# Optimization experiments

Hardware: AMD Instinct MI355X
Metric: run time of the kernel (lower is better)

## Reference

```python
import jax, jax.numpy as jnp
import numpy as np

DIM = 384
WS = 8        # window_size
SHIFT = 4     # shift_size
HEADS = 8
HEAD_DIM = DIM // HEADS
SCALE = HEAD_DIM ** (-0.5)
EPS = 1e-5


def layernorm(x, g, b):
    m = jnp.mean(x, axis=-1, keepdims=True)
    v = jnp.var(x, axis=-1, keepdims=True)
    return (x - m) * jax.lax.rsqrt(v + EPS) * g + b


def setup_inputs() -> dict:
    key = jax.random.key(0)
    ks = jax.random.split(key, 8)
    s = 0.02
    return {
        "x": jax.random.normal(ks[0], (8, DIM, 64, 64), dtype=jnp.float32),
        "qkv_w": jax.random.normal(ks[1], (DIM, 3 * DIM), dtype=jnp.float32) * s,
        "qkv_b": jnp.zeros((3 * DIM,), jnp.float32),
        "proj_w": jax.random.normal(ks[2], (DIM, DIM), dtype=jnp.float32) * s,
        "proj_b": jnp.zeros((DIM,), jnp.float32),
        "ln1_g": jnp.ones((DIM,), jnp.float32),
        "ln1_b": jnp.zeros((DIM,), jnp.float32),
        "ln2_g": jnp.ones((DIM,), jnp.float32),
        "ln2_b": jnp.zeros((DIM,), jnp.float32),
        "mlp_w1": jax.random.normal(ks[3], (DIM, 4 * DIM), dtype=jnp.float32) * s,
        "mlp_b1": jnp.zeros((4 * DIM,), jnp.float32),
        "mlp_w2": jax.random.normal(ks[4], (4 * DIM, DIM), dtype=jnp.float32) * s,
        "mlp_b2": jnp.zeros((DIM,), jnp.float32),
    }


def reference(x, qkv_w, qkv_b, proj_w, proj_b, ln1_g, ln1_b, ln2_g, ln2_b,
              mlp_w1, mlp_b1, mlp_w2, mlp_b2):
    B, C, H, W = x.shape
    x_skip = jnp.transpose(x, (0, 2, 3, 1))  # [B,H,W,C]
    xh = x_skip
    pad_b = (-H) % WS
    pad_r = (-W) % WS
    xh = jnp.pad(xh, ((0, 0), (0, pad_b), (0, pad_r), (0, 0)))
    Hp, Wp = xh.shape[1], xh.shape[2]
    if SHIFT > 0:
        xh = jnp.roll(xh, (-SHIFT, -SHIFT), axis=(1, 2))
    # window partition -> [B*nH*nW, WS*WS, C]
    win = xh.reshape(B, Hp // WS, WS, Wp // WS, WS, C)
    win = win.transpose(0, 1, 3, 2, 4, 5).reshape(-1, WS * WS, C)
    win = layernorm(win, ln1_g, ln1_b)
    # windowed MHA (no shift mask in original module)
    Bw, N, _ = win.shape
    qkv = (win @ qkv_w + qkv_b).reshape(Bw, N, 3, HEADS, HEAD_DIM)
    qkv = qkv.transpose(2, 0, 3, 1, 4)  # [3, Bw, H, N, d]
    q, k, v = qkv[0] * SCALE, qkv[1], qkv[2]
    attn = jax.nn.softmax(jnp.einsum('bhnd,bhmd->bhnm', q, k), axis=-1)
    out = jnp.einsum('bhnm,bhmd->bhnd', attn, v)
    out = out.transpose(0, 2, 1, 3).reshape(Bw, N, C)
    out = out @ proj_w + proj_b
    # window reverse
    xh = out.reshape(B, Hp // WS, Wp // WS, WS, WS, C)
    xh = xh.transpose(0, 1, 3, 2, 4, 5).reshape(B, Hp, Wp, C)
    if SHIFT > 0:
        xh = jnp.roll(xh, (SHIFT, SHIFT), axis=(1, 2))
    xh = xh[:, :H, :W, :] + x_skip
    h = layernorm(xh, ln2_g, ln2_b)
    h = jax.nn.gelu(h @ mlp_w1 + mlp_b1, approximate=False) @ mlp_w2 + mlp_b2
    return jnp.transpose(h, (0, 3, 1, 2))  # [B,C,H,W]
```

## Files before the change

kernel.cpp:

```cpp
#include <hip/hip_runtime.h>
#include <hip/hip_bf16.h>
#include <math.h>

#define DIM   384
#define HEADS 8
#define HD    48
#define NTOK  32768
#define NWIN  512

typedef __attribute__((ext_vector_type(8))) short bf16x8;
typedef __attribute__((ext_vector_type(8))) unsigned short u16x8;
typedef __attribute__((ext_vector_type(4))) float f32x4;

__device__ __forceinline__ float bf2f(unsigned short u) {
    unsigned int v = ((unsigned int)u) << 16;
    return __uint_as_float(v);
}
__device__ __forceinline__ unsigned short f2bf(float f) {
    __bf16 b = (__bf16)f;
    return __builtin_bit_cast(unsigned short, b);
}

__device__ __forceinline__ float gelu(float v) {
    float z  = v * 0.70710678118654752f;
    float az = fabsf(z);
    float t  = __builtin_amdgcn_rcpf(1.0f + 0.47047f * az);
    float p  = t * (0.3480242f + t * (-0.0958798f + t * 0.7478556f));
    float ea = 1.0f - p * __expf(-az * az);
    float er = copysignf(ea, z);
    return 0.5f * v * (1.0f + er);
}

__device__ __forceinline__ void tok2src(int tok, int& b, int& hs, int& ws) {
    int bb  = tok >> 12;
    int win = (tok >> 6) & 63;
    int t   = tok & 63;
    int hi = win >> 3, wi = win & 7;
    int r  = t >> 3,  cc = t & 7;
    b  = bb;
    hs = (hi * 8 + r  + 4) & 63;
    ws = (wi * 8 + cc + 4) & 63;
}

__global__ __launch_bounds__(256) void k_wt4(const float* __restrict__ qkv_w,
                                             const float* __restrict__ proj_w,
                                             const float* __restrict__ w1,
                                             const float* __restrict__ w2,
                                             unsigned short* __restrict__ d0,
                                             unsigned short* __restrict__ d1,
                                             unsigned short* __restrict__ d2,
                                             unsigned short* __restrict__ d3) {
    __shared__ unsigned short T[64][66];
    int b = blockIdx.x;
    const float* W; unsigned short* Wt; int K, N, lt;
    if (b < 108)      { W = qkv_w;  Wt = d0; K = 384;  N = 1152; lt = b; }
    else if (b < 144) { W = proj_w; Wt = d1; K = 384;  N = 384;  lt = b - 108; }
    else if (b < 288) { W = w1;     Wt = d2; K = 384;  N = 1536; lt = b - 144; }
    else              { W = w2;     Wt = d3; K = 1536; N = 384;  lt = b - 288; }
    int tn = N >> 6;
    int k0 = (lt / tn) << 6, n0 = (lt % tn) << 6;
    int t  = threadIdx.x;
    int cl = t & 63, rw = t >> 6;
    #pragma unroll
    for (int p = 0; p < 16; p++) {
        int kk = p * 4 + rw;
        T[cl][kk] = f2bf(W[(size_t)(k0 + kk) * N + n0 + cl]);
    }
    __syncthreads();
    #pragma unroll
    for (int p = 0; p < 16; p++) {
        int nn = p * 4 + rw;
        Wt[(size_t)(n0 + nn) * K + k0 + cl] = T[nn][cl];
    }
}

__global__ __launch_bounds__(256) void k_ln1(const float* __restrict__ x,
                                             const float* __restrict__ g,
                                             const float* __restrict__ bt,
                                             unsigned short* __restrict__ ln1) {
    int blk = blockIdx.x;
    int b  = blk >> 6, hs = blk & 63;
    int t  = threadIdx.x;
    int w  = t & 63, cg = t >> 6;
    const float* row = x + (size_t)b * DIM * 4096 + hs * 64;

    float sum = 0.f, sq = 0.f;
    for (int i = 0; i < 96; i++) {
        int c = i * 4 + cg;
        float v = row[(size_t)c * 4096 + w];
        sum += v; sq += v * v;
    }
    __shared__ float red[2][4][64];
    __shared__ float mean_s[64], rstd_s[64];
    red[0][cg][w] = sum; red[1][cg][w] = sq;
    __syncthreads();
    if (t < 64) {
        float s  = red[0][0][t] + red[0][1][t] + red[0][2][t] + red[0][3][t];
        float q2 = red[1][0][t] + red[1][1][t] + red[1][2][t] + red[1][3][t];
        float mean = s * (1.0f / DIM);
        float var  = q2 * (1.0f / DIM) - mean * mean;
        mean_s[t] = mean;
        rstd_s[t] = rsqrtf(var + 1e-5f);
    }
    __syncthreads();

    int wp = t >> 2, seg = t & 3;
    int hr = (hs + 60) & 63, wr = (wp + 60) & 63;
    int tok = ((b * 8 + (hr >> 3)) * 8 + (wr >> 3)) * 64 + (hr & 7) * 8 + (wr & 7);

    __shared__ __align__(16) unsigned short tile[64][72];
    for (int chunk = 0; chunk < 6; chunk++) {
        float mean = mean_s[w], rstd = rstd_s[w];
        #pragma unroll
        for (int it = 0; it < 16; it++) {
            int cl = it * 4 + cg;
            int c  = chunk * 64 + cl;
            float v = row[(size_t)c * 4096 + w];
            tile[w][cl] = f2bf((v - mean) * rstd * g[c] + bt[c]);
        }
        __syncthreads();
        u16x8 v0 = *(const u16x8*)&tile[wp][seg * 16];
        u16x8 v1 = *(const u16x8*)&tile[wp][seg * 16 + 8];
        unsigned short* op = ln1 + (size_t)tok * DIM + chunk * 64 + seg * 16;
        *(u16x8*)op = v0;
        *(u16x8*)(op + 8) = v1;
        __syncthreads();
    }
}

template <int EPI>
__global__ __launch_bounds__(256) void k_gemm_mfma(
        const unsigned short* __restrict__ A,
        const unsigned short* __restrict__ Bt,
        const float* __restrict__ bias,
        void* __restrict__ Cout,
        const float* __restrict__ xres,
        int N, int K, int GX) {
    __shared__ __align__(16) unsigned short SH[24576];
    int tid  = threadIdx.x;
    int lane = tid & 63;
    int wave = tid >> 6;
    int wm = wave >> 1, wn = wave & 1;
    int quad = lane >> 4, l15 = lane & 15;

    int l   = blockIdx.x;
    int xcd = l & 7;
    int r_  = l >> 3;
    int bx  = r_ % GX;
    int by  = (r_ / GX) * 8 + xcd;
    int m0 = by * 128, n0 = bx * 128;

    const unsigned short* gA0 = A  + (size_t)(m0 +      lane) * K + wave * 8;
    const unsigned short* gA1 = A  + (size_t)(m0 + 64 + lane) * K + wave * 8;
    const unsigned short* gB0 = Bt + (size_t)(n0 +      lane) * K + wave * 8;
    const unsigned short* gB1 = Bt + (size_t)(n0 + 64 + lane) * K + wave * 8;

    auto stage = [&](int buf) {
        __builtin_amdgcn_global_load_lds(
            (const __attribute__((address_space(1))) void*)gA0,
            (__attribute__((address_space(3))) void*)&SH[buf * 4096 + wave * 1024],
            16, 0, 0);
        __builtin_amdgcn_global_load_lds(
            (const __attribute__((address_space(1))) void*)gA1,
            (__attribute__((address_space(3))) void*)&SH[buf * 4096 + wave * 1024 + 512],
            16, 0, 0);
        __builtin_amdgcn_global_load_lds(
            (const __attribute__((address_space(1))) void*)gB0,
            (__attribute__((address_space(3))) void*)&SH[12288 + buf * 4096 + wave * 1024],
            16, 0, 0);
        __builtin_amdgcn_global_load_lds(
            (const __attribute__((address_space(1))) void*)gB1,
            (__attribute__((address_space(3))) void*)&SH[12288 + buf * 4096 + wave * 1024 + 512],
            16, 0, 0);
        gA0 += 32; gA1 += 32; gB0 += 32; gB1 += 32;
    };

    f32x4 acc[4][4] = {};
    int nsteps = K >> 5;

    stage(0);
    stage(1);
    int cur = 0, nxt = 2;
    for (int t = 0; t < nsteps; ++t) {
        __builtin_amdgcn_s_barrier();
        if (t + 2 < nsteps) {
            stage(nxt);
            if (++nxt == 3) nxt = 0;
            asm volatile("s_waitcnt vmcnt(8)" ::: "memory");
        } else if (t + 2 == nsteps) {
            asm volatile("s_waitcnt vmcnt(4)" ::: "memory");
        } else {
            asm volatile("s_waitcnt vmcnt(0)" ::: "memory");
        }
        __builtin_amdgcn_s_barrier();

        bf16x8 af[4], bfr[4];
        #pragma unroll
        for (int r = 0; r < 4; r++)
            af[r] = *(const bf16x8*)&SH[cur * 4096 + (quad * 128 + wm * 64 + r * 16 + l15) * 8];
        #pragma unroll
        for (int r2 = 0; r2 < 4; r2++)
            bfr[r2] = *(const bf16x8*)&SH[12288 + cur * 4096 + (quad * 128 + wn * 64 + r2 * 16 + l15) * 8];
        #pragma unroll
        for (int r = 0; r < 4; r++)
            #pragma unroll
            for (int r2 = 0; r2 < 4; r2++)
                acc[r][r2] = __builtin_amdgcn_mfma_f32_16x16x32_bf16(
                                 af[r], bfr[r2], acc[r][r2], 0, 0, 0);
        if (++cur == 3) cur = 0;
    }

    if (EPI == 2 || EPI == 3) {
        #pragma unroll
        for (int r2 = 0; r2 < 4; r2++) {
            int n = n0 + wn * 64 + r2 * 16 + l15;
            float bn = bias[n];
            #pragma unroll
            for (int r = 0; r < 4; r++) {
                #pragma unroll
                for (int reg = 0; reg < 4; reg++) {
                    int m = m0 + wm * 64 + r * 16 + quad * 4 + reg;
                    float v = acc[r][r2][reg] + bn;
                    if (EPI == 2) {
                        int b, hs, ws_;
                        tok2src(m, b, hs, ws_);
                        v += xres[(((size_t)b * DIM + n) * 64 + hs) * 64 + ws_];
                        int p = (b * 64 + hs) * 64 + ws_;
                        ((float*)Cout)[(size_t)p * N + n] = v;
                    } else {
                        ((float*)Cout)[(size_t)m * N + n] = v;
                    }
                }
            }
        }
    } else if (EPI == 5) {
        float* SF = (float*)SH;
        __syncthreads();
        int b   = m0 >> 12;
        int hs0 = (m0 >> 6) & 63;
        #pragma unroll
        for (int h2 = 0; h2 < 2; h2++) {
            if (wm == h2) {
                #pragma unroll
                for (int r2 = 0; r2 < 4; r2++) {
                    int c = wn * 64 + r2 * 16 + l15;
                    float bn = bias[n0 + c];
                    #pragma unroll
                    for (int r = 0; r < 4; r++) {
                        f32x4 v4;
                        #pragma unroll
                        for (int reg = 0; reg < 4; reg++)
                            v4[reg] = acc[r][r2][reg] + bn;
                        *(f32x4*)&SF[c * 68 + r * 16 + quad * 4] = v4;
                    }
                }
            }
            __syncthreads();
            #pragma unroll
            for (int i = 0; i < 8; i++) {
                int id = tid + i * 256;
                int c  = id >> 4, ch = id & 15;
                f32x4 v = *(const f32x4*)&SF[c * 68 + ch * 4];
                float* dst = (float*)Cout + ((size_t)(b * DIM + n0 + c) * 64 + hs0 + h2) * 64;
                *(f32x4*)&dst[ch * 4] = v;
            }
            __syncthreads();
        }
    } else {
        __syncthreads();
        #pragma unroll
        for (int r2 = 0; r2 < 4; r2++) {
            int col = wn * 64 + r2 * 16 + l15;
            float bn = bias[n0 + col];
            #pragma unroll
            for (int r = 0; r < 4; r++) {
                int row0 = wm * 64 + r * 16 + quad * 4;
                #pragma unroll
                for (int reg = 0; reg < 4; reg++) {
                    int row = row0 + reg;
                    float v = acc[r][r2][reg] + bn;
                    if (EPI == 1) v = gelu(v);
                    SH[(row * 136 + col) ^ (((row >> 3) & 1) << 4)] = f2bf(v);
                }
            }
        }
        __syncthreads();
        #pragma unroll
        for (int i = 0; i < 8; i++) {
            int chunk = tid + i * 256;
            int m = chunk >> 4, nc = chunk & 15;
            int idx = (m * 136 + nc * 8) ^ (((m >> 3) & 1) << 4);
            u16x8 v = *(const u16x8*)&SH[idx];
            if (EPI == 4) {
                int n = n0 + nc * 8;
                int qi  = n / 384;
                int rem = n - qi * 384;
                int hh  = rem / 48;
                int d   = rem - hh * 48;
                *(u16x8*)&((unsigned short*)Cout)[((size_t)(qi * 8 + hh) * NTOK + m0 + m) * 48 + d] = v;
            } else {
                *(u16x8*)&((unsigned short*)Cout)[(size_t)(m0 + m) * N + n0 + nc * 8] = v;
            }
        }
    }
}

__global__ __launch_bounds__(256) void k_attn_mfma(
        const unsigned short* __restrict__ qkvh,
        unsigned short* __restrict__ attn) {
    __shared__ __align__(16) unsigned short lds[4][8064];
    int tid  = threadIdx.x;
    int lane = tid & 63;
    int wave = tid >> 6;
    int quad = lane >> 4, l15 = lane & 15;
    int win  = blockIdx.x;
    int tok0 = win * 64;
    unsigned short* VT = &lds[wave][0];
    unsigned short* P  = &lds[wave][3456];
    const float scale = 0.14433756729740643f;

    for (int hi = 0; hi < 2; hi++) {
        int h = wave + hi * 4;
        const unsigned short* qb = qkvh + ((size_t)(0 * 8 + h) * NTOK + tok0) * 48;
        const unsigned short* kb = qkvh + ((size_t)(1 * 8 + h) * NTOK + tok0) * 48;
        const unsigned short* vb = qkvh + ((size_t)(2 * 8 + h) * NTOK + tok0) * 48;

        #pragma unroll
        for (int i = 0; i < 6; i++) {
            u16x8 v = *(const u16x8*)&vb[lane * 48 + i * 8];
            #pragma unroll
            for (int j = 0; j < 8; j++)
                VT[(i * 8 + j) * 72 + lane] = v[j];
        }

        bf16x8 kf[4][2];
        #pragma unroll
        for (int ni = 0; ni < 4; ni++) {
            kf[ni][0] = *(const bf16x8*)&kb[(ni * 16 + l15) * 48 + quad * 8];
            bf16x8 z = {};
            if (quad < 2)
                z = *(const bf16x8*)&kb[(ni * 16 + l15) * 48 + 32 + quad * 8];
            kf[ni][1] = z;
        }

        f32x4 sacc[4][4] = {};
        #pragma unroll
        for (int mi = 0; mi < 4; mi++) {
            bf16x8 qf0 = *(const bf16x8*)&qb[(mi * 16 + l15) * 48 + quad * 8];
            bf16x8 qf1 = {};
            if (quad < 2)
                qf1 = *(const bf16x8*)&qb[(mi * 16 + l15) * 48 + 32 + quad * 8];
            #pragma unroll
            for (int ni = 0; ni < 4; ni++) {
                sacc[mi][ni] = __builtin_amdgcn_mfma_f32_16x16x32_bf16(qf0, kf[ni][0], sacc[mi][ni], 0, 0, 0);
                sacc[mi][ni] = __builtin_amdgcn_mfma_f32_16x16x32_bf16(qf1, kf[ni][1], sacc[mi][ni], 0, 0, 0);
            }
        }

        #pragma unroll
        for (int mi = 0; mi < 4; mi++) {
            #pragma unroll
            for (int reg = 0; reg < 4; reg++) {
                float s0 = sacc[mi][0][reg] * scale;
                float s1 = sacc[mi][1][reg] * scale;
                float s2 = sacc[mi][2][reg] * scale;
                float s3 = sacc[mi][3][reg] * scale;
                float mx = fmaxf(fmaxf(s0, s1), fmaxf(s2, s3));
                #pragma unroll
                for (int off = 1; off < 16; off <<= 1)
                    mx = fmaxf(mx, __shfl_xor(mx, off));
                float e0 = __expf(s0 - mx);
                float e1 = __expf(s1 - mx);
                float e2 = __expf(s2 - mx);
                float e3 = __expf(s3 - mx);
                float sm = e0 + e1 + e2 + e3;
                #pragma unroll
                for (int off = 1; off < 16; off <<= 1)
                    sm += __shfl_xor(sm, off);
                float inv = 1.0f / sm;
                int row = mi * 16 + quad * 4 + reg;
                P[row * 72 +  0 + l15] = f2bf(e0 * inv);
                P[row * 72 + 16 + l15] = f2bf(e1 * inv);
                P[row * 72 + 32 + l15] = f2bf(e2 * inv);
                P[row * 72 + 48 + l15] = f2bf(e3 * inv);
            }
        }

        bf16x8 vf[3][2];
        #pragma unroll
        for (int ni = 0; ni < 3; ni++)
            #pragma unroll
            for (int kt = 0; kt < 2; kt++)
                vf[ni][kt] = *(const bf16x8*)&VT[(ni * 16 + l15) * 72 + kt * 32 + quad * 8];

        #pragma unroll
        for (int mi = 0; mi < 4; mi++) {
            bf16x8 pf0 = *(const bf16x8*)&P[(mi * 16 + l15) * 72 + quad * 8];
            bf16x8 pf1 = *(const bf16x8*)&P[(mi * 16 + l15) * 72 + 32 + quad * 8];
            f32x4 o[3] = {};
            #pragma unroll
            for (int ni = 0; ni < 3; ni++) {
                o[ni] = __builtin_amdgcn_mfma_f32_16x16x32_bf16(pf0, vf[ni][0], o[ni], 0, 0, 0);
                o[ni] = __builtin_amdgcn_mfma_f32_16x16x32_bf16(pf1, vf[ni][1], o[ni], 0, 0, 0);
            }
            #pragma unroll
            for (int ni = 0; ni < 3; ni++)
                #pragma unroll
                for (int reg = 0; reg < 4; reg++) {
                    int tok = tok0 + mi * 16 + quad * 4 + reg;
                    attn[(size_t)tok * DIM + h * HD + ni * 16 + l15] = f2bf(o[ni][reg]);
                }
        }
    }
}

__global__ __launch_bounds__(64) void k_ln2(const float* __restrict__ y,
                                            const float* __restrict__ g,
                                            const float* __restrict__ bt,
                                            unsigned short* __restrict__ out) {
    int tok = blockIdx.x;
    int t   = threadIdx.x;
    const float* row = y + (size_t)tok * DIM;
    float v[6];
    float sum = 0.f, sq = 0.f;
    #pragma unroll
    for (int i = 0; i < 6; i++) {
        v[i] = row[i * 64 + t];
        sum += v[i]; sq += v[i] * v[i];
    }
    #pragma unroll
    for (int o = 32; o > 0; o >>= 1) {
        sum += __shfl_xor(sum, o, 64);
        sq  += __shfl_xor(sq, o, 64);
    }
    float mean = sum * (1.0f / DIM);
    float var  = sq * (1.0f / DIM) - mean * mean;
    float rstd = rsqrtf(var + 1e-5f);
    unsigned short* orow = out + (size_t)tok * DIM;
    #pragma unroll
    for (int i = 0; i < 6; i++) {
        int c = i * 64 + t;
        orow[c] = f2bf((v[i] - mean) * rstd * g[c] + bt[c]);
    }
}

extern "C" void kernel_launch(void* const* d_in, const int* in_sizes, int n_in,
                              void* d_out, int out_size, void* d_ws, size_t ws_size,
                              hipStream_t stream) {
    const float* x      = (const float*)d_in[0];
    const float* qkv_w  = (const float*)d_in[1];
    const float* qkv_b  = (const float*)d_in[2];
    const float* proj_w = (const float*)d_in[3];
    const float* proj_b = (const float*)d_in[4];
    const float* ln1_g  = (const float*)d_in[5];
    const float* ln1_b  = (const float*)d_in[6];
    const float* ln2_g  = (const float*)d_in[7];
    const float* ln2_b  = (const float*)d_in[8];
    const float* w1     = (const float*)d_in[9];
    const float* b1     = (const float*)d_in[10];
    const float* w2     = (const float*)d_in[11];
    const float* b2     = (const float*)d_in[12];

    char* ws = (char*)d_ws;
    unsigned short* qkv_wt  = (unsigned short*)(ws + 0);
    unsigned short* proj_wt = (unsigned short*)(ws + 884736);
    unsigned short* w1t     = (unsigned short*)(ws + 1179648);
    unsigned short* w2t     = (unsigned short*)(ws + 2359296);
    unsigned short* ln1     = (unsigned short*)(ws + 4194304);
    unsigned short* qkv     = (unsigned short*)(ws + 29360128);
    unsigned short* attn    = (unsigned short*)(ws + 104857600);
    float*          y       = (float*)(ws + 130023424);
    unsigned short* ln2     = ln1;
    unsigned short* mid     = qkv;

    k_wt4<<<432, 256, 0, stream>>>(qkv_w, proj_w, w1, w2, qkv_wt, proj_wt, w1t, w2t);
    k_ln1<<<512, 256, 0, stream>>>(x, ln1_g, ln1_b, ln1);
    k_gemm_mfma<4><<<9 * 256, 256, 0, stream>>>(ln1, qkv_wt, qkv_b, qkv, nullptr, 1152, 384, 9);
    k_attn_mfma<<<NWIN, 256, 0, stream>>>(qkv, attn);
    k_gemm_mfma<2><<<3 * 256, 256, 0, stream>>>(attn, proj_wt, proj_b, y, x, 384, 384, 3);
    k_ln2<<<NTOK, 64, 0, stream>>>(y, ln2_g, ln2_b, ln2);
    k_gemm_mfma<1><<<12 * 256, 256, 0, stream>>>(ln2, w1t, b1, mid, nullptr, 1536, 384, 12);
    k_gemm_mfma<5><<<3 * 256, 256, 0, stream>>>(mid, w2t, b2, (float*)d_out, nullptr, 384, 1536, 3);
}
```

Measured before the change: 459.1 us.

## Add 256x128 GEMM tile variant for QKV and MLP1 projections

Adds an MT template parameter so the GEMM kernel can compute a 256-row by 128-column tile per block. Each B fragment loaded from LDS is reused across twice as many MFMAs, and the grid for the QKV and MLP-up GEMMs is halved. The new path double-buffers instead of triple-buffering and keeps two accumulator sets, which raises register pressure and may lower occupancy. The two GEMMs whose epilogues do the layout transposes stay on the 128x128 path.

Result: slower. 495.3 us (+7.9%).

```diff
diff --git a/kernel.cpp b/kernel.cpp
--- a/kernel.cpp
+++ b/kernel.cpp
@@ -128,7 +128,7 @@
     }
 }
 
-template <int EPI>
+template <int EPI, int MT>
 __global__ __launch_bounds__(256) void k_gemm_mfma(
         const unsigned short* __restrict__ A,
         const unsigned short* __restrict__ Bt,
@@ -148,69 +148,13 @@
     int r_  = l >> 3;
     int bx  = r_ % GX;
     int by  = (r_ / GX) * 8 + xcd;
-    int m0 = by * 128, n0 = bx * 128;
-
-    const unsigned short* gA0 = A  + (size_t)(m0 +      lane) * K + wave * 8;
-    const unsigned short* gA1 = A  + (size_t)(m0 + 64 + lane) * K + wave * 8;
-    const unsigned short* gB0 = Bt + (size_t)(n0 +      lane) * K + wave * 8;
-    const unsigned short* gB1 = Bt + (size_t)(n0 + 64 + lane) * K + wave * 8;
-
-    auto stage = [&](int buf) {
-        __builtin_amdgcn_global_load_lds(
-            (const __attribute__((address_space(1))) void*)gA0,
-            (__attribute__((address_space(3))) void*)&SH[buf * 4096 + wave * 1024],
-            16, 0, 0);
-        __builtin_amdgcn_global_load_lds(
-            (const __attribute__((address_space(1))) void*)gA1,
-            (__attribute__((address_space(3))) void*)&SH[buf * 4096 + wave * 1024 + 512],
-            16, 0, 0);
-        __builtin_amdgcn_global_load_lds(
-            (const __attribute__((address_space(1))) void*)gB0,
-            (__attribute__((address_space(3))) void*)&SH[12288 + buf * 4096 + wave * 1024],
-            16, 0, 0);
-        __builtin_amdgcn_global_load_lds(
-            (const __attribute__((address_space(1))) void*)gB1,
-            (__attribute__((address_space(3))) void*)&SH[12288 + buf * 4096 + wave * 1024 + 512],
-            16, 0, 0);
-        gA0 += 32; gA1 += 32; gB0 += 32; gB1 += 32;
-    };
-
-    f32x4 acc[4][4] = {};
+    int m0 = by * 128 * MT, n0 = bx * 128;
+
+    f32x4 acc0[4][4] = {};
+    f32x4 acc1[4][4] = {};
     int nsteps = K >> 5;
 
-    stage(0);
-    stage(1);
-    int cur = 0, nxt = 2;
-    for (int t = 0; t < nsteps; ++t) {
-        __builtin_amdgcn_s_barrier();
-        if (t + 2 < nsteps) {
-            stage(nxt);
-            if (++nxt == 3) nxt = 0;
-            asm volatile("s_waitcnt vmcnt(8)" ::: "memory");
-        } else if (t + 2 == nsteps) {
-            asm volatile("s_waitcnt vmcnt(4)" ::: "memory");
-        } else {
-            asm volatile("s_waitcnt vmcnt(0)" ::: "memory");
-        }
-        __builtin_amdgcn_s_barrier();
-
-        bf16x8 af[4], bfr[4];
-        #pragma unroll
-        for (int r = 0; r < 4; r++)
-            af[r] = *(const bf16x8*)&SH[cur * 4096 + (quad * 128 + wm * 64 + r * 16 + l15) * 8];
-        #pragma unroll
-        for (int r2 = 0; r2 < 4; r2++)
-            bfr[r2] = *(const bf16x8*)&SH[12288 + cur * 4096 + (quad * 128 + wn * 64 + r2 * 16 + l15) * 8];
-        #pragma unroll
-        for (int r = 0; r < 4; r++)
-            #pragma unroll
-            for (int r2 = 0; r2 < 4; r2++)
-                acc[r][r2] = __builtin_amdgcn_mfma_f32_16x16x32_bf16(
-                                 af[r], bfr[r2], acc[r][r2], 0, 0, 0);
-        if (++cur == 3) cur = 0;
-    }
-
-    if (EPI == 2 || EPI == 3) {
+    auto epi_f32 = [&](const f32x4 (&acc)[4][4], int m0h) {
         #pragma unroll
         for (int r2 = 0; r2 < 4; r2++) {
             int n = n0 + wn * 64 + r2 * 16 + l15;
@@ -219,7 +163,7 @@
             for (int r = 0; r < 4; r++) {
                 #pragma unroll
                 for (int reg = 0; reg < 4; reg++) {
-                    int m = m0 + wm * 64 + r * 16 + quad * 4 + reg;
+                    int m = m0h + wm * 64 + r * 16 + quad * 4 + reg;
                     float v = acc[r][r2][reg] + bn;
                     if (EPI == 2) {
                         int b, hs, ws_;
@@ -233,40 +177,8 @@
                 }
             }
         }
-    } else if (EPI == 5) {
-        float* SF = (float*)SH;
-        __syncthreads();
-        int b   = m0 >> 12;
-        int hs0 = (m0 >> 6) & 63;
-        #pragma unroll
-        for (int h2 = 0; h2 < 2; h2++) {
-            if (wm == h2) {
-                #pragma unroll
-                for (int r2 = 0; r2 < 4; r2++) {
-                    int c = wn * 64 + r2 * 16 + l15;
-                    float bn = bias[n0 + c];
-                    #pragma unroll
-                    for (int r = 0; r < 4; r++) {
-                        f32x4 v4;
-                        #pragma unroll
-                        for (int reg = 0; reg < 4; reg++)
-                            v4[reg] = acc[r][r2][reg] + bn;
-                        *(f32x4*)&SF[c * 68 + r * 16 + quad * 4] = v4;
-                    }
-                }
-            }
-            __syncthreads();
-            #pragma unroll
-            for (int i = 0; i < 8; i++) {
-                int id = tid + i * 256;
-                int c  = id >> 4, ch = id & 15;
-                f32x4 v = *(const f32x4*)&SF[c * 68 + ch * 4];
-                float* dst = (float*)Cout + ((size_t)(b * DIM + n0 + c) * 64 + hs0 + h2) * 64;
-                *(f32x4*)&dst[ch * 4] = v;
-            }
-            __syncthreads();
-        }
-    } else {
+    };
+    auto epi_bf16 = [&](const f32x4 (&acc)[4][4], int m0h) {
         __syncthreads();
         #pragma unroll
         for (int r2 = 0; r2 < 4; r2++) {
@@ -297,11 +209,168 @@
                 int rem = n - qi * 384;
                 int hh  = rem / 48;
                 int d   = rem - hh * 48;
-                *(u16x8*)&((unsigned short*)Cout)[((size_t)(qi * 8 + hh) * NTOK + m0 + m) * 48 + d] = v;
+                *(u16x8*)&((unsigned short*)Cout)[((size_t)(qi * 8 + hh) * NTOK + m0h + m) * 48 + d] = v;
             } else {
-                *(u16x8*)&((unsigned short*)Cout)[(size_t)(m0 + m) * N + n0 + nc * 8] = v;
-            }
-        }
+                *(u16x8*)&((unsigned short*)Cout)[(size_t)(m0h + m) * N + n0 + nc * 8] = v;
+            }
+        }
+    };
+
+    if constexpr (MT == 1) {
+        const unsigned short* gA0 = A  + (size_t)(m0 +      lane) * K + wave * 8;
+        const unsigned short* gA1 = A  + (size_t)(m0 + 64 + lane) * K + wave * 8;
+        const unsigned short* gB0 = Bt + (size_t)(n0 +      lane) * K + wave * 8;
+        const unsigned short* gB1 = Bt + (size_t)(n0 + 64 + lane) * K + wave * 8;
+        auto stage = [&](int buf) {
+            __builtin_amdgcn_global_load_lds(
+                (const __attribute__((address_space(1))) void*)gA0,
+                (__attribute__((address_space(3))) void*)&SH[buf * 4096 + wave * 1024], 16, 0, 0);
+            __builtin_amdgcn_global_load_lds(
+                (const __attribute__((address_space(1))) void*)gA1,
+                (__attribute__((address_space(3))) void*)&SH[buf * 4096 + wave * 1024 + 512], 16, 0, 0);
+            __builtin_amdgcn_global_load_lds(
+                (const __attribute__((address_space(1))) void*)gB0,
+                (__attribute__((address_space(3))) void*)&SH[12288 + buf * 4096 + wave * 1024], 16, 0, 0);
+            __builtin_amdgcn_global_load_lds(
+                (const __attribute__((address_space(1))) void*)gB1,
+                (__attribute__((address_space(3))) void*)&SH[12288 + buf * 4096 + wave * 1024 + 512], 16, 0, 0);
+            gA0 += 32; gA1 += 32; gB0 += 32; gB1 += 32;
+        };
+        stage(0);
+        stage(1);
+        int cur = 0, nxt = 2;
+        for (int t = 0; t < nsteps; ++t) {
+            __builtin_amdgcn_s_barrier();
+            if (t + 2 < nsteps) {
+                stage(nxt);
+                if (++nxt == 3) nxt = 0;
+                asm volatile("s_waitcnt vmcnt(8)" ::: "memory");
+            } else if (t + 2 == nsteps) {
+                asm volatile("s_waitcnt vmcnt(4)" ::: "memory");
+            } else {
+                asm volatile("s_waitcnt vmcnt(0)" ::: "memory");
+            }
+            __builtin_amdgcn_s_barrier();
+
+            bf16x8 af[4], bfr[4];
+            #pragma unroll
+            for (int r = 0; r < 4; r++)
+                af[r] = *(const bf16x8*)&SH[cur * 4096 + (quad * 128 + wm * 64 + r * 16 + l15) * 8];
+            #pragma unroll
+            for (int r2 = 0; r2 < 4; r2++)
+                bfr[r2] = *(const bf16x8*)&SH[12288 + cur * 4096 + (quad * 128 + wn * 64 + r2 * 16 + l15) * 8];
+            #pragma unroll
+            for (int r = 0; r < 4; r++)
+                #pragma unroll
+                for (int r2 = 0; r2 < 4; r2++)
+                    acc0[r][r2] = __builtin_amdgcn_mfma_f32_16x16x32_bf16(
+                                     af[r], bfr[r2], acc0[r][r2], 0, 0, 0);
+            if (++cur == 3) cur = 0;
+        }
+    } else {
+        const unsigned short* gA0 = A  + (size_t)(m0 +       lane) * K + wave * 8;
+        const unsigned short* gA1 = A  + (size_t)(m0 +  64 + lane) * K + wave * 8;
+        const unsigned short* gA2 = A  + (size_t)(m0 + 128 + lane) * K + wave * 8;
+        const unsigned short* gA3 = A  + (size_t)(m0 + 192 + lane) * K + wave * 8;
+        const unsigned short* gB0 = Bt + (size_t)(n0 +       lane) * K + wave * 8;
+        const unsigned short* gB1 = Bt + (size_t)(n0 +  64 + lane) * K + wave * 8;
+        auto stage2 = [&](int buf) {
+            __builtin_amdgcn_global_load_lds(
+                (const __attribute__((address_space(1))) void*)gA0,
+                (__attribute__((address_space(3))) void*)&SH[buf * 8192 + wave * 2048], 16, 0, 0);
+            __builtin_amdgcn_global_load_lds(
+                (const __attribute__((address_space(1))) void*)gA1,
+                (__attribute__((address_space(3))) void*)&SH[buf * 8192 + wave * 2048 + 512], 16, 0, 0);
+            __builtin_amdgcn_global_load_lds(
+                (const __attribute__((address_space(1))) void*)gA2,
+                (__attribute__((address_space(3))) void*)&SH[buf * 8192 + wave * 2048 + 1024], 16, 0, 0);
+            __builtin_amdgcn_global_load_lds(
+                (const __attribute__((address_space(1))) void*)gA3,
+                (__attribute__((address_space(3))) void*)&SH[buf * 8192 + wave * 2048 + 1536], 16, 0, 0);
+            __builtin_amdgcn_global_load_lds(
+                (const __attribute__((address_space(1))) void*)gB0,
+                (__attribute__((address_space(3))) void*)&SH[16384 + buf * 4096 + wave * 1024], 16, 0, 0);
+            __builtin_amdgcn_global_load_lds(
+                (const __attribute__((address_space(1))) void*)gB1,
+                (__attribute__((address_space(3))) void*)&SH[16384 + buf * 4096 + wave * 1024 + 512], 16, 0, 0);
+            gA0 += 32; gA1 += 32; gA2 += 32; gA3 += 32; gB0 += 32; gB1 += 32;
+        };
+        stage2(0);
+        for (int t = 0; t < nsteps; ++t) {
+            int cur = t & 1;
+            __builtin_amdgcn_s_barrier();
+            if (t + 1 < nsteps) {
+                stage2(cur ^ 1);
+                asm volatile("s_waitcnt vmcnt(6)" ::: "memory");
+            } else {
+                asm volatile("s_waitcnt vmcnt(0)" ::: "memory");
+            }
+            __builtin_amdgcn_s_barrier();
+
+            bf16x8 a0[4], a1[4], bfr[4];
+            #pragma unroll
+            for (int r2 = 0; r2 < 4; r2++)
+                bfr[r2] = *(const bf16x8*)&SH[16384 + cur * 4096 + (quad * 128 + wn * 64 + r2 * 16 + l15) * 8];
+            #pragma unroll
+            for (int r = 0; r < 4; r++)
+                a0[r] = *(const bf16x8*)&SH[cur * 8192 + (quad * 256 + wm * 64 + r * 16 + l15) * 8];
+            #pragma unroll
+            for (int r = 0; r < 4; r++)
+                a1[r] = *(const bf16x8*)&SH[cur * 8192 + (quad * 256 + 128 + wm * 64 + r * 16 + l15) * 8];
+            #pragma unroll
+            for (int r = 0; r < 4; r++)
+                #pragma unroll
+                for (int r2 = 0; r2 < 4; r2++)
+                    acc0[r][r2] = __builtin_amdgcn_mfma_f32_16x16x32_bf16(
+                                     a0[r], bfr[r2], acc0[r][r2], 0, 0, 0);
+            #pragma unroll
+            for (int r = 0; r < 4; r++)
+                #pragma unroll
+                for (int r2 = 0; r2 < 4; r2++)
+                    acc1[r][r2] = __builtin_amdgcn_mfma_f32_16x16x32_bf16(
+                                     a1[r], bfr[r2], acc1[r][r2], 0, 0, 0);
+        }
+    }
+
+    if constexpr (EPI == 2 || EPI == 3) {
+        epi_f32(acc0, m0);
+        if constexpr (MT == 2) epi_f32(acc1, m0 + 128);
+    } else if constexpr (EPI == 5) {
+        float* SF = (float*)SH;
+        __syncthreads();
+        int b   = m0 >> 12;
+        int hs0 = (m0 >> 6) & 63;
+        #pragma unroll
+        for (int h2 = 0; h2 < 2; h2++) {
+            if (wm == h2) {
+                #pragma unroll
+                for (int r2 = 0; r2 < 4; r2++) {
+                    int c = wn * 64 + r2 * 16 + l15;
+                    float bn = bias[n0 + c];
+                    #pragma unroll
+                    for (int r = 0; r < 4; r++) {
+                        f32x4 v4;
+                        #pragma unroll
+                        for (int reg = 0; reg < 4; reg++)
+                            v4[reg] = acc0[r][r2][reg] + bn;
+                        *(f32x4*)&SF[c * 68 + r * 16 + quad * 4] = v4;
+                    }
+                }
+            }
+            __syncthreads();
+            #pragma unroll
+            for (int i = 0; i < 8; i++) {
+                int id = tid + i * 256;
+                int c  = id >> 4, ch = id & 15;
+                f32x4 v = *(const f32x4*)&SF[c * 68 + ch * 4];
+                float* dst = (float*)Cout + ((size_t)(b * DIM + n0 + c) * 64 + hs0 + h2) * 64;
+                *(f32x4*)&dst[ch * 4] = v;
+            }
+            __syncthreads();
+        }
+    } else {
+        epi_bf16(acc0, m0);
+        if constexpr (MT == 2) epi_bf16(acc1, m0 + 128);
     }
 }
 
@@ -475,10 +544,10 @@
 
     k_wt4<<<432, 256, 0, stream>>>(qkv_w, proj_w, w1, w2, qkv_wt, proj_wt, w1t, w2t);
     k_ln1<<<512, 256, 0, stream>>>(x, ln1_g, ln1_b, ln1);
-    k_gemm_mfma<4><<<9 * 256, 256, 0, stream>>>(ln1, qkv_wt, qkv_b, qkv, nullptr, 1152, 384, 9);
+    k_gemm_mfma<4, 2><<<128 * 9, 256, 0, stream>>>(ln1, qkv_wt, qkv_b, qkv, nullptr, 1152, 384, 9);
     k_attn_mfma<<<NWIN, 256, 0, stream>>>(qkv, attn);
-    k_gemm_mfma<2><<<3 * 256, 256, 0, stream>>>(attn, proj_wt, proj_b, y, x, 384, 384, 3);
+    k_gemm_mfma<2, 1><<<3 * 256, 256, 0, stream>>>(attn, proj_wt, proj_b, y, x, 384, 384, 3);
     k_ln2<<<NTOK, 64, 0, stream>>>(y, ln2_g, ln2_b, ln2);
-    k_gemm_mfma<1><<<12 * 256, 256, 0, stream>>>(ln2, w1t, b1, mid, nullptr, 1536, 384, 12);
-    k_gemm_mfma<5><<<3 * 256, 256, 0, stream>>>(mid, w2t, b2, (float*)d_out, nullptr, 384, 1536, 3);
-}
+    k_gemm_mfma<1, 2><<<128 * 12, 256, 0, stream>>>(ln2, w1t, b1, mid, nullptr, 1536, 384, 12);
+    k_gemm_mfma<5, 1><<<3 * 256, 256, 0, stream>>>(mid, w2t, b2, (float*)d_out, nullptr, 384, 1536, 3);
+}
```

## Replace 4-wave 128x128 GEMM blocks with single-wave 64x64 blocks

Applied to the files above, without the earlier changes.

Rewrites the shared GEMM kernel so each workgroup is one wavefront computing a 64x64 tile. Staging becomes double-buffered instead of triple-buffered, and all barriers are dropped, since one wave needs no cross-wave sync. The goal is to remove barrier overhead and raise the block count and occupancy. The cost is that each A/B tile loaded into LDS is reused only within a 64x64 tile, so global and L2 traffic roughly doubles, and the LDS read patterns lose their XOR swizzle.

Measured after the change: 817.6 us. +78.1%, slower.

```diff
diff --git a/kernel.cpp b/kernel.cpp
--- a/kernel.cpp
+++ b/kernel.cpp
@@ -129,18 +129,15 @@
 }
 
 template <int EPI>
-__global__ __launch_bounds__(256) void k_gemm_mfma(
+__global__ __launch_bounds__(64) void k_gemm_wave(
         const unsigned short* __restrict__ A,
         const unsigned short* __restrict__ Bt,
         const float* __restrict__ bias,
         void* __restrict__ Cout,
         const float* __restrict__ xres,
         int N, int K, int GX) {
-    __shared__ __align__(16) unsigned short SH[24576];
-    int tid  = threadIdx.x;
-    int lane = tid & 63;
-    int wave = tid >> 6;
-    int wm = wave >> 1, wn = wave & 1;
+    __shared__ __align__(16) unsigned short SH[8704];
+    int lane = threadIdx.x;
     int quad = lane >> 4, l15 = lane & 15;
 
     int l   = blockIdx.x;
@@ -148,78 +145,65 @@
     int r_  = l >> 3;
     int bx  = r_ % GX;
     int by  = (r_ / GX) * 8 + xcd;
-    int m0 = by * 128, n0 = bx * 128;
-
-    const unsigned short* gA0 = A  + (size_t)(m0 +      lane) * K + wave * 8;
-    const unsigned short* gA1 = A  + (size_t)(m0 + 64 + lane) * K + wave * 8;
-    const unsigned short* gB0 = Bt + (size_t)(n0 +      lane) * K + wave * 8;
-    const unsigned short* gB1 = Bt + (size_t)(n0 + 64 + lane) * K + wave * 8;
+    int m0 = by * 64, n0 = bx * 64;
+
+    const unsigned short* gA = A  + (size_t)(m0 + lane) * K;
+    const unsigned short* gB = Bt + (size_t)(n0 + lane) * K;
+    int k0 = 0;
 
     auto stage = [&](int buf) {
-        __builtin_amdgcn_global_load_lds(
-            (const __attribute__((address_space(1))) void*)gA0,
-            (__attribute__((address_space(3))) void*)&SH[buf * 4096 + wave * 1024],
-            16, 0, 0);
-        __builtin_amdgcn_global_load_lds(
-            (const __attribute__((address_space(1))) void*)gA1,
-            (__attribute__((address_space(3))) void*)&SH[buf * 4096 + wave * 1024 + 512],
-            16, 0, 0);
-        __builtin_amdgcn_global_load_lds(
-            (const __attribute__((address_space(1))) void*)gB0,
-            (__attribute__((address_space(3))) void*)&SH[12288 + buf * 4096 + wave * 1024],
-            16, 0, 0);
-        __builtin_amdgcn_global_load_lds(
-            (const __attribute__((address_space(1))) void*)gB1,
-            (__attribute__((address_space(3))) void*)&SH[12288 + buf * 4096 + wave * 1024 + 512],
-            16, 0, 0);
-        gA0 += 32; gA1 += 32; gB0 += 32; gB1 += 32;
+        #pragma unroll
+        for (int j = 0; j < 4; j++)
+            __builtin_amdgcn_global_load_lds(
+                (const __attribute__((address_space(1))) void*)(gA + k0 + j * 8),
+                (__attribute__((address_space(3))) void*)&SH[buf * 4096 + j * 512],
+                16, 0, 0);
+        #pragma unroll
+        for (int j = 0; j < 4; j++)
+            __builtin_amdgcn_global_load_lds(
+                (const __attribute__((address_space(1))) void*)(gB + k0 + j * 8),
+                (__attribute__((address_space(3))) void*)&SH[buf * 4096 + 2048 + j * 512],
+                16, 0, 0);
+        k0 += 32;
     };
 
     f32x4 acc[4][4] = {};
     int nsteps = K >> 5;
 
     stage(0);
-    stage(1);
-    int cur = 0, nxt = 2;
     for (int t = 0; t < nsteps; ++t) {
-        __builtin_amdgcn_s_barrier();
-        if (t + 2 < nsteps) {
-            stage(nxt);
-            if (++nxt == 3) nxt = 0;
+        int cur = t & 1;
+        if (t + 1 < nsteps) {
+            stage(cur ^ 1);
             asm volatile("s_waitcnt vmcnt(8)" ::: "memory");
-        } else if (t + 2 == nsteps) {
-            asm volatile("s_waitcnt vmcnt(4)" ::: "memory");
         } else {
             asm volatile("s_waitcnt vmcnt(0)" ::: "memory");
         }
-        __builtin_amdgcn_s_barrier();
-
         bf16x8 af[4], bfr[4];
         #pragma unroll
         for (int r = 0; r < 4; r++)
-            af[r] = *(const bf16x8*)&SH[cur * 4096 + (quad * 128 + wm * 64 + r * 16 + l15) * 8];
+            af[r] = *(const bf16x8*)&SH[cur * 4096 + quad * 512 + (r * 16 + l15) * 8];
         #pragma unroll
         for (int r2 = 0; r2 < 4; r2++)
-            bfr[r2] = *(const bf16x8*)&SH[12288 + cur * 4096 + (quad * 128 + wn * 64 + r2 * 16 + l15) * 8];
+            bfr[r2] = *(const bf16x8*)&SH[cur * 4096 + 2048 + quad * 512 + (r2 * 16 + l15) * 8];
         #pragma unroll
         for (int r = 0; r < 4; r++)
             #pragma unroll
             for (int r2 = 0; r2 < 4; r2++)
                 acc[r][r2] = __builtin_amdgcn_mfma_f32_16x16x32_bf16(
                                  af[r], bfr[r2], acc[r][r2], 0, 0, 0);
-        if (++cur == 3) cur = 0;
-    }
-
-    if (EPI == 2 || EPI == 3) {
+    }
+
+    if constexpr (EPI == 2 || EPI == 3) {
         #pragma unroll
         for (int r2 = 0; r2 < 4; r2++) {
-            int n = n0 + wn * 64 + r2 * 16 + l15;
+            int n = n0 + r2 * 16 + l15;
             float bn = bias[n];
             #pragma unroll
             for (int r = 0; r < 4; r++) {
                 #pragma unroll
                 for (int reg = 0; reg < 4; reg++) {
-                    int m = m0 + wm * 64 + r * 16 + quad * 4 + reg;
+                    int m = m0 + r * 16 + quad * 4 + reg;
                     float v = acc[r][r2][reg] + bn;
                     if (EPI == 2) {
                         int b, hs, ws_;
@@ -233,73 +217,61 @@
                 }
             }
         }
-    } else if (EPI == 5) {
+    } else if constexpr (EPI == 5) {
         float* SF = (float*)SH;
-        __syncthreads();
-        int b   = m0 >> 12;
-        int hs0 = (m0 >> 6) & 63;
-        #pragma unroll
-        for (int h2 = 0; h2 < 2; h2++) {
-            if (wm == h2) {
-                #pragma unroll
-                for (int r2 = 0; r2 < 4; r2++) {
-                    int c = wn * 64 + r2 * 16 + l15;
-                    float bn = bias[n0 + c];
-                    #pragma unroll
-                    for (int r = 0; r < 4; r++) {
-                        f32x4 v4;
-                        #pragma unroll
-                        for (int reg = 0; reg < 4; reg++)
-                            v4[reg] = acc[r][r2][reg] + bn;
-                        *(f32x4*)&SF[c * 68 + r * 16 + quad * 4] = v4;
-                    }
-                }
-            }
-            __syncthreads();
-            #pragma unroll
-            for (int i = 0; i < 8; i++) {
-                int id = tid + i * 256;
-                int c  = id >> 4, ch = id & 15;
-                f32x4 v = *(const f32x4*)&SF[c * 68 + ch * 4];
-                float* dst = (float*)Cout + ((size_t)(b * DIM + n0 + c) * 64 + hs0 + h2) * 64;
-                *(f32x4*)&dst[ch * 4] = v;
-            }
-            __syncthreads();
+        int b  = m0 >> 12;
+        int hs = (m0 >> 6) & 63;
+        #pragma unroll
+        for (int r2 = 0; r2 < 4; r2++) {
+            int c = r2 * 16 + l15;
+            float bn = bias[n0 + c];
+            #pragma unroll
+            for (int r = 0; r < 4; r++) {
+                f32x4 v4;
+                #pragma unroll
+                for (int reg = 0; reg < 4; reg++)
+                    v4[reg] = acc[r][r2][reg] + bn;
+                *(f32x4*)&SF[c * 65 + r * 16 + quad * 4] = v4;
+            }
+        }
+        #pragma unroll
+        for (int i = 0; i < 16; i++) {
+            int id = i * 64 + lane;
+            int c  = id >> 4, ch = id & 15;
+            f32x4 v = *(const f32x4*)&SF[c * 65 + ch * 4];
+            float* dst = (float*)Cout + ((size_t)(b * DIM + n0 + c) * 64 + hs) * 64;
+            *(f32x4*)&dst[ch * 4] = v;
         }
     } else {
-        __syncthreads();
         #pragma unroll
         for (int r2 = 0; r2 < 4; r2++) {
-            int col = wn * 64 + r2 * 16 + l15;
+            int col = r2 * 16 + l15;
             float bn = bias[n0 + col];
             #pragma unroll
             for (int r = 0; r < 4; r++) {
-                int row0 = wm * 64 + r * 16 + quad * 4;
+                int row0 = r * 16 + quad * 4;
                 #pragma unroll
                 for (int reg = 0; reg < 4; reg++) {
-                    int row = row0 + reg;
                     float v = acc[r][r2][reg] + bn;
                     if (EPI == 1) v = gelu(v);
-                    SH[(row * 136 + col) ^ (((row >> 3) & 1) << 4)] = f2bf(v);
+                    SH[(row0 + reg) * 68 + col] = f2bf(v);
                 }
             }
         }
-        __syncthreads();
         #pragma unroll
         for (int i = 0; i < 8; i++) {
-            int chunk = tid + i * 256;
-            int m = chunk >> 4, nc = chunk & 15;
-            int idx = (m * 136 + nc * 8) ^ (((m >> 3) & 1) << 4);
-            u16x8 v = *(const u16x8*)&SH[idx];
+            int m  = i * 8 + (lane >> 3);
+            int ch = lane & 7;
+            u16x8 v = *(const u16x8*)&SH[m * 68 + ch * 8];
             if (EPI == 4) {
-                int n = n0 + nc * 8;
+                int n = n0 + ch * 8;
                 int qi  = n / 384;
                 int rem = n - qi * 384;
                 int hh  = rem / 48;
                 int d   = rem - hh * 48;
                 *(u16x8*)&((unsigned short*)Cout)[((size_t)(qi * 8 + hh) * NTOK + m0 + m) * 48 + d] = v;
             } else {
-                *(u16x8*)&((unsigned short*)Cout)[(size_t)(m0 + m) * N + n0 + nc * 8] = v;
+                *(u16x8*)&((unsigned short*)Cout)[(size_t)(m0 + m) * N + n0 + ch * 8] = v;
             }
         }
     }
@@ -475,10 +447,10 @@
 
     k_wt4<<<432, 256, 0, stream>>>(qkv_w, proj_w, w1, w2, qkv_wt, proj_wt, w1t, w2t);
     k_ln1<<<512, 256, 0, stream>>>(x, ln1_g, ln1_b, ln1);
-    k_gemm_mfma<4><<<9 * 256, 256, 0, stream>>>(ln1, qkv_wt, qkv_b, qkv, nullptr, 1152, 384, 9);
+    k_gemm_wave<4><<<512 * 18, 64, 0, stream>>>(ln1, qkv_wt, qkv_b, qkv, nullptr, 1152, 384, 18);
     k_attn_mfma<<<NWIN, 256, 0, stream>>>(qkv, attn);
-    k_gemm_mfma<2><<<3 * 256, 256, 0, stream>>>(attn, proj_wt, proj_b, y, x, 384, 384, 3);
+    k_gemm_wave<2><<<512 * 6, 64, 0, stream>>>(attn, proj_wt, proj_b, y, x, 384, 384, 6);
     k_ln2<<<NTOK, 64, 0, stream>>>(y, ln2_g, ln2_b, ln2);
-    k_gemm_mfma<1><<<12 * 256, 256, 0, stream>>>(ln2, w1t, b1, mid, nullptr, 1536, 384, 12);
-    k_gemm_mfma<5><<<3 * 256, 256, 0, stream>>>(mid, w2t, b2, (float*)d_out, nullptr, 384, 1536, 3);
-}
+    k_gemm_wave<1><<<512 * 24, 64, 0, stream>>>(ln2, w1t, b1, mid, nullptr, 1536, 384, 24);
+    k_gemm_wave<5><<<512 * 6, 64, 0, stream>>>(mid, w2t, b2, (float*)d_out, nullptr, 384, 1536, 6);
+}
```
